# Kernel optimization log

Measured on AMD Instinct MI355X. Metric: run time of the kernel, lower is better.

## Reference

```python
import jax, jax.numpy as jnp
import numpy as np

B, S, D = 8, 1024, 512          # batch, seq_len, embed_dim
H = 8                            # num_heads
KD = D                           # key_dim = embed_dim (per source)
DM = H * KD                      # internal d_model = 4096
FF = 2048                        # dense_dim
EPS = 1e-3                       # keras LayerNormalization default epsilon


def glorot(key, shape):
    fan_in, fan_out = shape[0], shape[1]
    lim = np.sqrt(6.0 / (fan_in + fan_out)).astype(np.float32)
    return jax.random.uniform(key, shape, jnp.float32, -lim, lim)


def setup_inputs() -> dict:
    key = jax.random.key(0)
    ks = jax.random.split(key, 8)
    return {
        "inputs": jax.random.normal(ks[0], (B, S, D), jnp.float32),
        "w_q": glorot(ks[1], (D, DM)), "b_q": jnp.zeros((DM,), jnp.float32),
        "w_k": glorot(ks[2], (D, DM)), "b_k": jnp.zeros((DM,), jnp.float32),
        "w_v": glorot(ks[3], (D, DM)), "b_v": jnp.zeros((DM,), jnp.float32),
        "w_o": glorot(ks[4], (DM, D)), "b_o": jnp.zeros((D,), jnp.float32),
        "w1": glorot(ks[5], (D, FF)), "b1": jnp.zeros((FF,), jnp.float32),
        "w2": glorot(ks[6], (FF, D)), "b2": jnp.zeros((D,), jnp.float32),
        "g1": jnp.ones((D,), jnp.float32), "beta1": jnp.zeros((D,), jnp.float32),
        "g2": jnp.ones((D,), jnp.float32), "beta2": jnp.zeros((D,), jnp.float32),
    }


def _layernorm(x, gamma, beta):
    mu = jnp.mean(x, axis=-1, keepdims=True)
    var = jnp.mean(jnp.square(x - mu), axis=-1, keepdims=True)
    return (x - mu) * jax.lax.rsqrt(var + EPS) * gamma + beta


def reference(inputs, w_q, b_q, w_k, b_k, w_v, b_v, w_o, b_o,
              w1, b1, w2, b2, g1, beta1, g2, beta2):
    # --- custom multi-head self-attention ---
    q = (inputs @ w_q + b_q).reshape(B, S, H, KD)   # [B,S,H,KD]
    k = (inputs @ w_k + b_k).reshape(B, S, H, KD)
    v = (inputs @ w_v + b_v).reshape(B, S, H, KD)
    scale = jnp.sqrt(jnp.float32(KD))
    scores = jnp.einsum("bqhd,bkhd->bhqk", q, k) / scale   # [B,H,S,S]
    attn = jax.nn.softmax(scores, axis=-1)
    ctx = jnp.einsum("bhqk,bkhd->bqhd", attn, v).reshape(B, S, DM)
    attn_out = ctx @ w_o + b_o                               # [B,S,D]
    # --- residual + LN 1 ---
    proj_in = _layernorm(inputs + attn_out, g1, beta1)
    # --- FFN ---
    ffn = jax.nn.relu(proj_in @ w1 + b1) @ w2 + b2
    # --- residual + LN 2 ---
    return _layernorm(proj_in + ffn, g2, beta2)
```

## Files before the change

kernel.cpp:

```cpp
#include <hip/hip_runtime.h>
#include <stdint.h>

typedef __bf16 bf16_t;
typedef bf16_t bf16x8 __attribute__((ext_vector_type(8)));
typedef float floatx4 __attribute__((ext_vector_type(4)));

__device__ __forceinline__ unsigned short f2bf(float f) {
  union { float f; uint32_t u; } v; v.f = f;
  return (unsigned short)((v.u + 0x7fffu + ((v.u >> 16) & 1u)) >> 16);
}

#define GLD16(g, l)                                                            \
  __builtin_amdgcn_global_load_lds(                                            \
      (const __attribute__((address_space(1))) void*)(g),                      \
      (__attribute__((address_space(3))) void*)(l), 16, 0, 0)

template <int BIAS_MODE, bool RELU, bool OUT_BF16, bool HAS_RESID>
__global__ __launch_bounds__(256) void gemm_bt(
    const unsigned short* __restrict__ A, const unsigned short* __restrict__ Bt,
    void* __restrict__ C, const float* __restrict__ bias,
    const float* __restrict__ resid, int K, int lda, int ldb, int ldc,
    long sA, long sB, long sC, long sR) {
  __shared__ unsigned short As[128 * 64];
  __shared__ unsigned short Bs[128 * 64];
  const int tid = threadIdx.x;
  const int lane = tid & 63;
  const int wave = tid >> 6;
  const unsigned short* Ab = A + blockIdx.z * sA + (long)blockIdx.y * 128 * lda;
  const unsigned short* Bb = Bt + blockIdx.z * sB + (long)blockIdx.x * 128 * ldb;
  const int wm = (wave & 1) << 6;
  const int wn = (wave >> 1) << 6;

  floatx4 acc[4][4] = {};

  const int sr = tid >> 3;
  const int sc = tid & 7;

  for (int kt = 0; kt < K; kt += 64) {
#pragma unroll
    for (int i = 0; i < 4; ++i) {
      int r = sr + i * 32;
      int gc = sc ^ (r & 7);
      GLD16(Ab + (long)r * lda + kt + gc * 8, As + (i * 256 + wave * 64) * 8);
    }
#pragma unroll
    for (int i = 0; i < 4; ++i) {
      int r = sr + i * 32;
      int gc = sc ^ (r & 7);
      GLD16(Bb + (long)r * ldb + kt + gc * 8, Bs + (i * 256 + wave * 64) * 8);
    }
    __syncthreads();
#pragma unroll
    for (int ks = 0; ks < 2; ++ks) {
      bf16x8 af[4], bfr[4];
#pragma unroll
      for (int i = 0; i < 4; ++i) {
        int row = wm + i * 16 + (lane & 15);
        int ch = (ks * 4 + (lane >> 4)) ^ (row & 7);
        af[i] = *(const bf16x8*)(As + row * 64 + ch * 8);
      }
#pragma unroll
      for (int j = 0; j < 4; ++j) {
        int row = wn + j * 16 + (lane & 15);
        int ch = (ks * 4 + (lane >> 4)) ^ (row & 7);
        bfr[j] = *(const bf16x8*)(Bs + row * 64 + ch * 8);
      }
#pragma unroll
      for (int i = 0; i < 4; ++i)
#pragma unroll
        for (int j = 0; j < 4; ++j)
          acc[i][j] = __builtin_amdgcn_mfma_f32_16x16x32_bf16(af[i], bfr[j],
                                                              acc[i][j], 0, 0, 0);
    }
    __syncthreads();
  }

  const int rl = (lane >> 4) << 2;
  const int cl = lane & 15;
#pragma unroll
  for (int i = 0; i < 4; ++i) {
#pragma unroll
    for (int j = 0; j < 4; ++j) {
#pragma unroll
      for (int rg = 0; rg < 4; ++rg) {
        int row = (blockIdx.y << 7) + wm + i * 16 + rl + rg;
        int col = (blockIdx.x << 7) + wn + j * 16 + cl;
        float v = acc[i][j][rg];
        if (BIAS_MODE == 1) v += bias[col];
        if (BIAS_MODE == 2) v += bias[row];
        if (HAS_RESID) v += resid[blockIdx.z * sR + (long)row * ldc + col];
        if (RELU) v = fmaxf(v, 0.0f);
        long idx = blockIdx.z * sC + (long)row * ldc + col;
        if (OUT_BF16)
          ((unsigned short*)C)[idx] = f2bf(v);
        else
          ((float*)C)[idx] = v;
      }
    }
  }
}

__global__ __launch_bounds__(512, 2) void attn(
    const unsigned short* __restrict__ qk, const unsigned short* __restrict__ vt,
    unsigned short* __restrict__ ctx) {
  __shared__ unsigned short ldsK[2][32 * 512];
  __shared__ unsigned short ldsV[2][32 * 512];
  __shared__ unsigned short ldsP[128 * 40];
  __shared__ float ldsL[128];

  const int tid = threadIdx.x;
  const int lane = tid & 63;
  const int wave = tid >> 6;
  const int quad = lane >> 4;
  const int l15 = lane & 15;
  const int b = blockIdx.x >> 3;
  const int h = blockIdx.x & 7;
  const int qblk = blockIdx.y << 7;
  const float cs = 0.044194173824159216f * 1.4426950408889634f;

  bf16x8 qf[16];
  {
    const unsigned short* qp =
        qk + (long)(b * 1024 + qblk + wave * 16 + l15) * 8192 + h * 512 +
        (quad << 3);
#pragma unroll
    for (int ks = 0; ks < 16; ++ks) qf[ks] = *(const bf16x8*)(qp + ks * 32);
  }

  floatx4 o[32];
#pragma unroll
  for (int i = 0; i < 32; ++i) o[i] = floatx4{0.f, 0.f, 0.f, 0.f};
  floatx4 l_i = floatx4{0.f, 0.f, 0.f, 0.f};

  const int st_d = lane >> 2;
  const int st_kc = ((lane & 3) - (lane >> 3)) & 3;

  {
#pragma unroll
    for (int i = 0; i < 4; ++i) {
      int r = i * 8 + wave;
      int gc = (lane & ~7) | ((lane ^ r) & 7);
      GLD16(qk + (long)(b * 1024 + r) * 8192 + 4096 + h * 512 + gc * 8,
            ldsK[0] + r * 512);
    }
#pragma unroll
    for (int i = 0; i < 4; ++i) {
      int j = i * 8 + wave;
      GLD16(vt + (long)(b * 4096 + h * 512 + j * 16 + st_d) * 1024 + st_kc * 8,
            ldsV[0] + j * 512);
    }
  }
  __syncthreads();

  for (int kt = 0; kt < 32; ++kt) {
    const unsigned short* kb = ldsK[kt & 1];
    const unsigned short* vb = ldsV[kt & 1];
    if (kt + 1 < 32) {
#pragma unroll
      for (int i = 0; i < 4; ++i) {
        int r = i * 8 + wave;
        int gc = (lane & ~7) | ((lane ^ r) & 7);
        GLD16(qk + (long)(b * 1024 + (kt + 1) * 32 + r) * 8192 + 4096 +
                  h * 512 + gc * 8,
              ldsK[(kt + 1) & 1] + r * 512);
      }
#pragma unroll
      for (int i = 0; i < 4; ++i) {
        int j = i * 8 + wave;
        GLD16(vt + (long)(b * 4096 + h * 512 + j * 16 + st_d) * 1024 +
                  (kt + 1) * 32 + st_kc * 8,
              ldsV[(kt + 1) & 1] + j * 512);
      }
    }

    floatx4 s0 = floatx4{0.f, 0.f, 0.f, 0.f}, s1 = floatx4{0.f, 0.f, 0.f, 0.f};
#pragma unroll
    for (int ks = 0; ks < 16; ++ks) {
      int ch = ks * 4 + quad;
      int sw = (ch & ~7) | ((ch ^ l15) & 7);
      bf16x8 k0 = *(const bf16x8*)(kb + l15 * 512 + sw * 8);
      bf16x8 k1 = *(const bf16x8*)(kb + (16 + l15) * 512 + sw * 8);
      s0 = __builtin_amdgcn_mfma_f32_16x16x32_bf16(qf[ks], k0, s0, 0, 0, 0);
      s1 = __builtin_amdgcn_mfma_f32_16x16x32_bf16(qf[ks], k1, s1, 0, 0, 0);
    }

    {
      unsigned short* pw = ldsP + wave * 16 * 40;
      const int rb = quad << 2;
#pragma unroll
      for (int r = 0; r < 4; ++r) {
        float e0 = __builtin_amdgcn_exp2f(s0[r] * cs);
        float e1 = __builtin_amdgcn_exp2f(s1[r] * cs);
        l_i[r] += e0 + e1;
        pw[(rb + r) * 40 + l15] = f2bf(e0);
        pw[(rb + r) * 40 + 16 + l15] = f2bf(e1);
      }
    }
    asm volatile("s_waitcnt lgkmcnt(0)\n\ts_barrier" ::: "memory");

#pragma unroll
    for (int half = 0; half < 2; ++half) {
      bf16x8 pf[4];
#pragma unroll
      for (int q4 = 0; q4 < 4; ++q4)
        pf[q4] = *(const bf16x8*)(ldsP + ((half * 4 + q4) * 16 + l15) * 40 +
                                  (quad << 3));
#pragma unroll
      for (int db = 0; db < 4; ++db) {
        int n = wave * 4 + db;
        bf16x8 vf = *(const bf16x8*)(
            vb + n * 512 + (l15 * 4 + ((quad + (l15 >> 1)) & 3)) * 8);
#pragma unroll
        for (int q4 = 0; q4 < 4; ++q4)
          o[(half * 4 + q4) * 4 + db] = __builtin_amdgcn_mfma_f32_16x16x32_bf16(
              pf[q4], vf, o[(half * 4 + q4) * 4 + db], 0, 0, 0);
      }
    }
    __syncthreads();
  }

#pragma unroll
  for (int r = 0; r < 4; ++r) {
    float rs = l_i[r];
    rs += __shfl_xor(rs, 1);
    rs += __shfl_xor(rs, 2);
    rs += __shfl_xor(rs, 4);
    rs += __shfl_xor(rs, 8);
    if (l15 == 0) ldsL[wave * 16 + (quad << 2) + r] = rs;
  }
  __syncthreads();

#pragma unroll
  for (int qb = 0; qb < 8; ++qb) {
    floatx4 lv = *(const floatx4*)(ldsL + qb * 16 + (quad << 2));
    floatx4 inv;
#pragma unroll
    for (int r = 0; r < 4; ++r) inv[r] = 1.0f / lv[r];
#pragma unroll
    for (int db = 0; db < 4; ++db) {
#pragma unroll
      for (int r = 0; r < 4; ++r) {
        long row = (long)(b * 1024 + qblk + qb * 16 + (quad << 2) + r);
        ctx[row * 4096 + h * 512 + wave * 64 + db * 16 + l15] =
            f2bf(o[qb * 4 + db][r] * inv[r]);
      }
    }
  }
}

template <bool WB>
__global__ __launch_bounds__(256) void ln_reduce(
    const float* __restrict__ p, long sP, const float* __restrict__ bias,
    const float* __restrict__ resid, const float* __restrict__ gamma,
    const float* __restrict__ beta, float* __restrict__ of,
    unsigned short* __restrict__ ob) {
  const long row = blockIdx.x;
  const int c = threadIdx.x * 2;
  const float2 a0 = ((const float2*)(p + row * 512))[threadIdx.x];
  const float2 a1 = ((const float2*)(p + sP + row * 512))[threadIdx.x];
  const float2 a2 = ((const float2*)(p + 2 * sP + row * 512))[threadIdx.x];
  const float2 a3 = ((const float2*)(p + 3 * sP + row * 512))[threadIdx.x];
  const float2 rv = ((const float2*)(resid + row * 512))[threadIdx.x];
  const float x0 = a0.x + a1.x + a2.x + a3.x + bias[c] + rv.x;
  const float x1 = a0.y + a1.y + a2.y + a3.y + bias[c + 1] + rv.y;
  float s = x0 + x1;
  float ss = x0 * x0 + x1 * x1;
#pragma unroll
  for (int d = 1; d < 64; d <<= 1) {
    s += __shfl_xor(s, d);
    ss += __shfl_xor(ss, d);
  }
  __shared__ float ps[4], pq[4];
  const int wave = threadIdx.x >> 6;
  if ((threadIdx.x & 63) == 0) {
    ps[wave] = s;
    pq[wave] = ss;
  }
  __syncthreads();
  s = ps[0] + ps[1] + ps[2] + ps[3];
  ss = pq[0] + pq[1] + pq[2] + pq[3];
  const float mu = s * (1.0f / 512.0f);
  const float rstd = rsqrtf(ss * (1.0f / 512.0f) - mu * mu + 1e-3f);
  const float y0 = (x0 - mu) * rstd * gamma[c] + beta[c];
  const float y1 = (x1 - mu) * rstd * gamma[c + 1] + beta[c + 1];
  ((float2*)(of + row * 512))[threadIdx.x] = make_float2(y0, y1);
  if (WB) {
    ushort2 o2;
    o2.x = f2bf(y0);
    o2.y = f2bf(y1);
    ((ushort2*)(ob + row * 512))[threadIdx.x] = o2;
  }
}

__global__ __launch_bounds__(256) void cast_bf16(const float* __restrict__ in,
                                                 unsigned short* __restrict__ out,
                                                 int n) {
  int i = (blockIdx.x * 256 + threadIdx.x) * 4;
  if (i < n) {
    float4 v = *(const float4*)(in + i);
    ushort4 o;
    o.x = f2bf(v.x);
    o.y = f2bf(v.y);
    o.z = f2bf(v.z);
    o.w = f2bf(v.w);
    *(ushort4*)(out + i) = o;
  }
}

__global__ __launch_bounds__(256) void transpose_cast(const float* __restrict__ in,
                                                      unsigned short* __restrict__ out,
                                                      int R, int C) {
  __shared__ float tile[32][33];
  const int tx = threadIdx.x & 31, ty = threadIdx.x >> 5;
  const int c0 = blockIdx.x * 32, r0 = blockIdx.y * 32;
#pragma unroll
  for (int i = 0; i < 4; ++i)
    tile[ty + i * 8][tx] = in[(long)(r0 + ty + i * 8) * C + c0 + tx];
  __syncthreads();
#pragma unroll
  for (int i = 0; i < 4; ++i)
    out[(long)(c0 + ty + i * 8) * R + r0 + tx] = f2bf(tile[tx][ty + i * 8]);
}

extern "C" void kernel_launch(void* const* d_in, const int* in_sizes, int n_in,
                              void* d_out, int out_size, void* d_ws,
                              size_t ws_size, hipStream_t stream) {
  const float* x = (const float*)d_in[0];
  const float* w_q = (const float*)d_in[1];
  const float* b_q = (const float*)d_in[2];
  const float* w_k = (const float*)d_in[3];
  const float* b_k = (const float*)d_in[4];
  const float* w_v = (const float*)d_in[5];
  const float* b_v = (const float*)d_in[6];
  const float* w_o = (const float*)d_in[7];
  const float* b_o = (const float*)d_in[8];
  const float* w1 = (const float*)d_in[9];
  const float* b1 = (const float*)d_in[10];
  const float* w2 = (const float*)d_in[11];
  const float* b2 = (const float*)d_in[12];
  const float* g1 = (const float*)d_in[13];
  const float* be1 = (const float*)d_in[14];
  const float* g2 = (const float*)d_in[15];
  const float* be2 = (const float*)d_in[16];
  float* out = (float*)d_out;

  char* ws = (char*)d_ws;
  size_t off = 0;
  auto alloc = [&](size_t n) {
    char* p = ws + off;
    off += (n + 255) & ~(size_t)255;
    return p;
  };
  unsigned short* xb = (unsigned short*)alloc(8192ll * 512 * 2);
  unsigned short* wqk_t = (unsigned short*)alloc(8192ll * 512 * 2);
  unsigned short* wv_t = (unsigned short*)alloc(4096ll * 512 * 2);
  unsigned short* wo_t = (unsigned short*)alloc(512ll * 4096 * 2);
  unsigned short* w1_t = (unsigned short*)alloc(2048ll * 512 * 2);
  unsigned short* w2_t = (unsigned short*)alloc(512ll * 2048 * 2);
  float* bqk = (float*)alloc(8192ll * 4);
  unsigned short* qkb = (unsigned short*)alloc(4096ll * 8192 * 2);
  unsigned short* vtb = (unsigned short*)alloc(4ll * 4096 * 1024 * 2);
  unsigned short* ctxf = (unsigned short*)alloc(8192ll * 4096 * 2);
  float* proj = (float*)alloc(8192ll * 512 * 4);
  unsigned short* projb = xb;
  unsigned short* h1 = qkb;
  float* pOP = (float*)qkb;
  float* pF2 = (float*)ctxf;

  hipMemcpyAsync(bqk, b_q, 4096 * 4, hipMemcpyDeviceToDevice, stream);
  hipMemcpyAsync(bqk + 4096, b_k, 4096 * 4, hipMemcpyDeviceToDevice, stream);

  cast_bf16<<<4096, 256, 0, stream>>>(x, xb, 8192 * 512);
  transpose_cast<<<dim3(128, 16), 256, 0, stream>>>(w_q, wqk_t, 512, 4096);
  transpose_cast<<<dim3(128, 16), 256, 0, stream>>>(w_k, wqk_t + 4096ll * 512, 512, 4096);
  transpose_cast<<<dim3(128, 16), 256, 0, stream>>>(w_v, wv_t, 512, 4096);
  transpose_cast<<<dim3(16, 128), 256, 0, stream>>>(w_o, wo_t, 4096, 512);
  transpose_cast<<<dim3(64, 16), 256, 0, stream>>>(w1, w1_t, 512, 2048);
  transpose_cast<<<dim3(16, 64), 256, 0, stream>>>(w2, w2_t, 2048, 512);

  for (int g = 0; g < 2; ++g) {
    const unsigned short* xg = xb + (long)g * 4096 * 512;
    gemm_bt<1, false, true, false><<<dim3(64, 32, 1), 256, 0, stream>>>(
        xg, wqk_t, qkb, bqk, nullptr, 512, 512, 512, 8192, 0, 0, 0, 0);
    gemm_bt<2, false, true, false><<<dim3(8, 32, 4), 256, 0, stream>>>(
        wv_t, xg, vtb, b_v, nullptr, 512, 512, 512, 1024, 0, 1024ll * 512,
        4096ll * 1024, 0);
    attn<<<dim3(32, 8), 512, 0, stream>>>(qkb, vtb, ctxf + (long)g * 4096 * 4096);
  }
  gemm_bt<0, false, false, false><<<dim3(4, 64, 4), 256, 0, stream>>>(
      ctxf, wo_t, pOP, nullptr, nullptr, 1024, 4096, 4096, 512, 1024, 1024,
      8192ll * 512, 0);
  ln_reduce<true><<<8192, 256, 0, stream>>>(pOP, 8192ll * 512, b_o, x, g1, be1,
                                            proj, projb);
  gemm_bt<1, true, true, false><<<dim3(16, 64, 1), 256, 0, stream>>>(
      projb, w1_t, h1, b1, nullptr, 512, 512, 512, 2048, 0, 0, 0, 0);
  gemm_bt<0, false, false, false><<<dim3(4, 64, 4), 256, 0, stream>>>(
      h1, w2_t, pF2, nullptr, nullptr, 512, 2048, 2048, 512, 512, 512,
      8192ll * 512, 0);
  ln_reduce<false><<<8192, 256, 0, stream>>>(pF2, 8192ll * 512, b2, proj, g2,
                                             be2, out, nullptr);
}
```

Before: 561.2 us.

## Halve attention query tile and single-buffer K/V with staggered loads

The attention kernel now handles 64 query rows per block with 4 waves instead of 128 rows with 8 waves, which doubles the grid, and each wave covers 128 output columns. The K/V double buffers become single buffers. V for the current tile loads while QK^T runs, and K for the next tile loads during the PV step after the barrier, so the LDS footprint roughly halves. The aim is more resident blocks and better load overlap. In exchange, each K/V tile is reused by half as many queries, so global K/V traffic doubles, and the added barriers may expose latency.

```diff
diff --git a/kernel.cpp b/kernel.cpp
--- a/kernel.cpp
+++ b/kernel.cpp
@@ -100,13 +100,13 @@
   }
 }
 
-__global__ __launch_bounds__(512, 2) void attn(
+__global__ __launch_bounds__(256, 2) void attn(
     const unsigned short* __restrict__ qk, const unsigned short* __restrict__ vt,
     unsigned short* __restrict__ ctx) {
-  __shared__ unsigned short ldsK[2][32 * 512];
-  __shared__ unsigned short ldsV[2][32 * 512];
-  __shared__ unsigned short ldsP[128 * 40];
-  __shared__ float ldsL[128];
+  __shared__ unsigned short ldsK[32 * 512];
+  __shared__ unsigned short ldsV[32 * 512];
+  __shared__ unsigned short ldsP[64 * 40];
+  __shared__ float ldsL[64];
 
   const int tid = threadIdx.x;
   const int lane = tid & 63;
@@ -115,7 +115,7 @@
   const int l15 = lane & 15;
   const int b = blockIdx.x >> 3;
   const int h = blockIdx.x & 7;
-  const int qblk = blockIdx.y << 7;
+  const int qblk = blockIdx.y << 6;
   const float cs = 0.044194173824159216f * 1.4426950408889634f;
 
   bf16x8 qf[16];
@@ -137,40 +137,23 @@
 
   {
 #pragma unroll
-    for (int i = 0; i < 4; ++i) {
-      int r = i * 8 + wave;
+    for (int i = 0; i < 8; ++i) {
+      int r = i * 4 + wave;
       int gc = (lane & ~7) | ((lane ^ r) & 7);
       GLD16(qk + (long)(b * 1024 + r) * 8192 + 4096 + h * 512 + gc * 8,
-            ldsK[0] + r * 512);
-    }
-#pragma unroll
-    for (int i = 0; i < 4; ++i) {
-      int j = i * 8 + wave;
-      GLD16(vt + (long)(b * 4096 + h * 512 + j * 16 + st_d) * 1024 + st_kc * 8,
-            ldsV[0] + j * 512);
-    }
-  }
-  __syncthreads();
+            ldsK + r * 512);
+    }
+  }
 
   for (int kt = 0; kt < 32; ++kt) {
-    const unsigned short* kb = ldsK[kt & 1];
-    const unsigned short* vb = ldsV[kt & 1];
-    if (kt + 1 < 32) {
-#pragma unroll
-      for (int i = 0; i < 4; ++i) {
-        int r = i * 8 + wave;
-        int gc = (lane & ~7) | ((lane ^ r) & 7);
-        GLD16(qk + (long)(b * 1024 + (kt + 1) * 32 + r) * 8192 + 4096 +
-                  h * 512 + gc * 8,
-              ldsK[(kt + 1) & 1] + r * 512);
-      }
-#pragma unroll
-      for (int i = 0; i < 4; ++i) {
-        int j = i * 8 + wave;
-        GLD16(vt + (long)(b * 4096 + h * 512 + j * 16 + st_d) * 1024 +
-                  (kt + 1) * 32 + st_kc * 8,
-              ldsV[(kt + 1) & 1] + j * 512);
-      }
+    __syncthreads();
+
+#pragma unroll
+    for (int i = 0; i < 8; ++i) {
+      int j = i * 4 + wave;
+      GLD16(vt + (long)(b * 4096 + h * 512 + j * 16 + st_d) * 1024 + kt * 32 +
+                st_kc * 8,
+            ldsV + j * 512);
     }
 
     floatx4 s0 = floatx4{0.f, 0.f, 0.f, 0.f}, s1 = floatx4{0.f, 0.f, 0.f, 0.f};
@@ -178,8 +161,8 @@
     for (int ks = 0; ks < 16; ++ks) {
       int ch = ks * 4 + quad;
       int sw = (ch & ~7) | ((ch ^ l15) & 7);
-      bf16x8 k0 = *(const bf16x8*)(kb + l15 * 512 + sw * 8);
-      bf16x8 k1 = *(const bf16x8*)(kb + (16 + l15) * 512 + sw * 8);
+      bf16x8 k0 = *(const bf16x8*)(ldsK + l15 * 512 + sw * 8);
+      bf16x8 k1 = *(const bf16x8*)(ldsK + (16 + l15) * 512 + sw * 8);
       s0 = __builtin_amdgcn_mfma_f32_16x16x32_bf16(qf[ks], k0, s0, 0, 0, 0);
       s1 = __builtin_amdgcn_mfma_f32_16x16x32_bf16(qf[ks], k1, s1, 0, 0, 0);
     }
@@ -196,27 +179,33 @@
         pw[(rb + r) * 40 + 16 + l15] = f2bf(e1);
       }
     }
-    asm volatile("s_waitcnt lgkmcnt(0)\n\ts_barrier" ::: "memory");
-
-#pragma unroll
-    for (int half = 0; half < 2; ++half) {
-      bf16x8 pf[4];
+    asm volatile("s_waitcnt vmcnt(0) lgkmcnt(0)\n\ts_barrier" ::: "memory");
+
+    if (kt + 1 < 32) {
+#pragma unroll
+      for (int i = 0; i < 8; ++i) {
+        int r = i * 4 + wave;
+        int gc = (lane & ~7) | ((lane ^ r) & 7);
+        GLD16(qk + (long)(b * 1024 + (kt + 1) * 32 + r) * 8192 + 4096 +
+                  h * 512 + gc * 8,
+              ldsK + r * 512);
+      }
+    }
+
+    bf16x8 pf[4];
+#pragma unroll
+    for (int q4 = 0; q4 < 4; ++q4)
+      pf[q4] = *(const bf16x8*)(ldsP + (q4 * 16 + l15) * 40 + (quad << 3));
+#pragma unroll
+    for (int db = 0; db < 8; ++db) {
+      int n = wave * 8 + db;
+      bf16x8 vf = *(const bf16x8*)(
+          ldsV + n * 512 + (l15 * 4 + ((quad + (l15 >> 1)) & 3)) * 8);
 #pragma unroll
       for (int q4 = 0; q4 < 4; ++q4)
-        pf[q4] = *(const bf16x8*)(ldsP + ((half * 4 + q4) * 16 + l15) * 40 +
-                                  (quad << 3));
-#pragma unroll
-      for (int db = 0; db < 4; ++db) {
-        int n = wave * 4 + db;
-        bf16x8 vf = *(const bf16x8*)(
-            vb + n * 512 + (l15 * 4 + ((quad + (l15 >> 1)) & 3)) * 8);
-#pragma unroll
-        for (int q4 = 0; q4 < 4; ++q4)
-          o[(half * 4 + q4) * 4 + db] = __builtin_amdgcn_mfma_f32_16x16x32_bf16(
-              pf[q4], vf, o[(half * 4 + q4) * 4 + db], 0, 0, 0);
-      }
-    }
-    __syncthreads();
+        o[q4 * 8 + db] = __builtin_amdgcn_mfma_f32_16x16x32_bf16(
+            pf[q4], vf, o[q4 * 8 + db], 0, 0, 0);
+    }
   }
 
 #pragma unroll
@@ -231,18 +220,18 @@
   __syncthreads();
 
 #pragma unroll
-  for (int qb = 0; qb < 8; ++qb) {
-    floatx4 lv = *(const floatx4*)(ldsL + qb * 16 + (quad << 2));
+  for (int q4 = 0; q4 < 4; ++q4) {
+    floatx4 lv = *(const floatx4*)(ldsL + q4 * 16 + (quad << 2));
     floatx4 inv;
 #pragma unroll
     for (int r = 0; r < 4; ++r) inv[r] = 1.0f / lv[r];
 #pragma unroll
-    for (int db = 0; db < 4; ++db) {
+    for (int db = 0; db < 8; ++db) {
 #pragma unroll
       for (int r = 0; r < 4; ++r) {
-        long row = (long)(b * 1024 + qblk + qb * 16 + (quad << 2) + r);
-        ctx[row * 4096 + h * 512 + wave * 64 + db * 16 + l15] =
-            f2bf(o[qb * 4 + db][r] * inv[r]);
+        long row = (long)(b * 1024 + qblk + q4 * 16 + (quad << 2) + r);
+        ctx[row * 4096 + h * 512 + wave * 128 + db * 16 + l15] =
+            f2bf(o[q4 * 8 + db][r] * inv[r]);
       }
     }
   }
@@ -385,7 +374,7 @@
     gemm_bt<2, false, true, false><<<dim3(8, 32, 4), 256, 0, stream>>>(
         wv_t, xg, vtb, b_v, nullptr, 512, 512, 512, 1024, 0, 1024ll * 512,
         4096ll * 1024, 0);
-    attn<<<dim3(32, 8), 512, 0, stream>>>(qkb, vtb, ctxf + (long)g * 4096 * 4096);
+    attn<<<dim3(32, 16), 256, 0, stream>>>(qkb, vtb, ctxf + (long)g * 4096 * 4096);
   }
   gemm_bt<0, false, false, false><<<dim3(4, 64, 4), 256, 0, stream>>>(
       ctxf, wo_t, pOP, nullptr, nullptr, 1024, 4096, 4096, 512, 1024, 1024,
```

New measurement: 572.1 us. Within noise of the previous version (+2.0%).

## Replace 128x128 GEMM with double-buffered 256x256 tile kernel using 8 waves

Applied to the files above, without the earlier changes.

Swaps the GEMM kernel for one that computes 256x256 output tiles with 512 threads. It double-buffers LDS so global-to-LDS loads for tile t+2 overlap the MFMA work on tile t, and raises wave priority around the MFMA bursts. Larger tiles raise arithmetic intensity and cut global traffic per FLOP. In exchange each block uses 128KB of LDS and more accumulator registers, and grids are smaller, which may lower occupancy and CU fill for the smaller GEMMs.

```diff
diff --git a/kernel.cpp b/kernel.cpp
--- a/kernel.cpp
+++ b/kernel.cpp
@@ -15,80 +15,115 @@
       (const __attribute__((address_space(1))) void*)(g),                      \
       (__attribute__((address_space(3))) void*)(l), 16, 0, 0)
 
-template <int BIAS_MODE, bool RELU, bool OUT_BF16, bool HAS_RESID>
-__global__ __launch_bounds__(256) void gemm_bt(
+template <int BIAS_MODE, bool RELU, bool OUT_BF16>
+__global__ __launch_bounds__(512, 2) void gemm256(
     const unsigned short* __restrict__ A, const unsigned short* __restrict__ Bt,
-    void* __restrict__ C, const float* __restrict__ bias,
-    const float* __restrict__ resid, int K, int lda, int ldb, int ldc,
-    long sA, long sB, long sC, long sR) {
-  __shared__ unsigned short As[128 * 64];
-  __shared__ unsigned short Bs[128 * 64];
+    void* __restrict__ C, const float* __restrict__ bias, int K, int lda,
+    int ldb, int ldc, long sA, long sB, long sC) {
+  __shared__ __align__(16) unsigned short As[2][256 * 64];
+  __shared__ __align__(16) unsigned short Bs[2][256 * 64];
   const int tid = threadIdx.x;
   const int lane = tid & 63;
   const int wave = tid >> 6;
-  const unsigned short* Ab = A + blockIdx.z * sA + (long)blockIdx.y * 128 * lda;
-  const unsigned short* Bb = Bt + blockIdx.z * sB + (long)blockIdx.x * 128 * ldb;
-  const int wm = (wave & 1) << 6;
+  const int quad = lane >> 4;
+  const int l15 = lane & 15;
+  const unsigned short* Ab = A + blockIdx.z * sA + (long)blockIdx.y * 256 * lda;
+  const unsigned short* Bb = Bt + blockIdx.z * sB + (long)blockIdx.x * 256 * ldb;
+  const int wm = (wave & 1) << 7;
   const int wn = (wave >> 1) << 6;
 
-  floatx4 acc[4][4] = {};
+  floatx4 acc[8][4] = {};
 
   const int sr = tid >> 3;
   const int sc = tid & 7;
-
-  for (int kt = 0; kt < K; kt += 64) {
+  const int NT = K >> 6;
+
+  auto stage = [&](int t, int buf) {
+    const int kt = t << 6;
 #pragma unroll
     for (int i = 0; i < 4; ++i) {
-      int r = sr + i * 32;
+      int r = sr + i * 64;
       int gc = sc ^ (r & 7);
-      GLD16(Ab + (long)r * lda + kt + gc * 8, As + (i * 256 + wave * 64) * 8);
+      GLD16(Ab + (long)r * lda + kt + gc * 8,
+            &As[buf][(i * 64 + (wave << 3)) * 64]);
     }
 #pragma unroll
     for (int i = 0; i < 4; ++i) {
-      int r = sr + i * 32;
+      int r = sr + i * 64;
       int gc = sc ^ (r & 7);
-      GLD16(Bb + (long)r * ldb + kt + gc * 8, Bs + (i * 256 + wave * 64) * 8);
-    }
-    __syncthreads();
-#pragma unroll
-    for (int ks = 0; ks < 2; ++ks) {
-      bf16x8 af[4], bfr[4];
-#pragma unroll
-      for (int i = 0; i < 4; ++i) {
-        int row = wm + i * 16 + (lane & 15);
-        int ch = (ks * 4 + (lane >> 4)) ^ (row & 7);
-        af[i] = *(const bf16x8*)(As + row * 64 + ch * 8);
-      }
-#pragma unroll
-      for (int j = 0; j < 4; ++j) {
-        int row = wn + j * 16 + (lane & 15);
-        int ch = (ks * 4 + (lane >> 4)) ^ (row & 7);
-        bfr[j] = *(const bf16x8*)(Bs + row * 64 + ch * 8);
-      }
-#pragma unroll
-      for (int i = 0; i < 4; ++i)
-#pragma unroll
-        for (int j = 0; j < 4; ++j)
-          acc[i][j] = __builtin_amdgcn_mfma_f32_16x16x32_bf16(af[i], bfr[j],
-                                                              acc[i][j], 0, 0, 0);
-    }
-    __syncthreads();
-  }
-
-  const int rl = (lane >> 4) << 2;
-  const int cl = lane & 15;
-#pragma unroll
-  for (int i = 0; i < 4; ++i) {
+      GLD16(Bb + (long)r * ldb + kt + gc * 8,
+            &Bs[buf][(i * 64 + (wave << 3)) * 64]);
+    }
+  };
+
+  stage(0, 0);
+  stage(1, 1);
+  asm volatile("s_waitcnt vmcnt(8)\n\ts_barrier" ::: "memory");
+
+  int cur = 0;
+  for (int t = 0; t < NT; ++t) {
+    const unsigned short* Ap = As[cur];
+    const unsigned short* Bp = Bs[cur];
+#pragma unroll
+    for (int ih = 0; ih < 2; ++ih) {
+      bf16x8 aF[4][2];
+#pragma unroll
+      for (int i4 = 0; i4 < 4; ++i4)
+#pragma unroll
+        for (int ks = 0; ks < 2; ++ks) {
+          int row = wm + ih * 64 + i4 * 16 + l15;
+          int sw = (ks * 4 + quad) ^ (row & 7);
+          aF[i4][ks] = *(const bf16x8*)(Ap + row * 64 + sw * 8);
+        }
+#pragma unroll
+      for (int jh = 0; jh < 2; ++jh) {
+        bf16x8 bF[2][2];
+#pragma unroll
+        for (int j2 = 0; j2 < 2; ++j2)
+#pragma unroll
+          for (int ks = 0; ks < 2; ++ks) {
+            int row = wn + jh * 32 + j2 * 16 + l15;
+            int sw = (ks * 4 + quad) ^ (row & 7);
+            bF[j2][ks] = *(const bf16x8*)(Bp + row * 64 + sw * 8);
+          }
+        __builtin_amdgcn_s_setprio(1);
+#pragma unroll
+        for (int j2 = 0; j2 < 2; ++j2)
+#pragma unroll
+          for (int i4 = 0; i4 < 4; ++i4)
+#pragma unroll
+            for (int ks = 0; ks < 2; ++ks)
+              acc[ih * 4 + i4][jh * 2 + j2] =
+                  __builtin_amdgcn_mfma_f32_16x16x32_bf16(
+                      aF[i4][ks], bF[j2][ks], acc[ih * 4 + i4][jh * 2 + j2],
+                      0, 0, 0);
+        __builtin_amdgcn_s_setprio(0);
+      }
+    }
+    if (t == NT - 1) break;
+    asm volatile("s_waitcnt lgkmcnt(0)\n\ts_barrier" ::: "memory");
+    if (t + 2 < NT) {
+      stage(t + 2, cur);
+      asm volatile("s_waitcnt vmcnt(8)\n\ts_barrier" ::: "memory");
+    } else {
+      asm volatile("s_waitcnt vmcnt(0)\n\ts_barrier" ::: "memory");
+    }
+    cur ^= 1;
+  }
+
+  const int rl = quad << 2;
+  const int cl = l15;
+#pragma unroll
+  for (int i = 0; i < 8; ++i) {
 #pragma unroll
     for (int j = 0; j < 4; ++j) {
 #pragma unroll
       for (int rg = 0; rg < 4; ++rg) {
-        int row = (blockIdx.y << 7) + wm + i * 16 + rl + rg;
-        int col = (blockIdx.x << 7) + wn + j * 16 + cl;
+        int row = (blockIdx.y << 8) + wm + i * 16 + rl + rg;
+        int col = (blockIdx.x << 8) + wn + j * 16 + cl;
         float v = acc[i][j][rg];
         if (BIAS_MODE == 1) v += bias[col];
         if (BIAS_MODE == 2) v += bias[row];
-        if (HAS_RESID) v += resid[blockIdx.z * sR + (long)row * ldc + col];
         if (RELU) v = fmaxf(v, 0.0f);
         long idx = blockIdx.z * sC + (long)row * ldc + col;
         if (OUT_BF16)
@@ -380,23 +415,22 @@
 
   for (int g = 0; g < 2; ++g) {
     const unsigned short* xg = xb + (long)g * 4096 * 512;
-    gemm_bt<1, false, true, false><<<dim3(64, 32, 1), 256, 0, stream>>>(
-        xg, wqk_t, qkb, bqk, nullptr, 512, 512, 512, 8192, 0, 0, 0, 0);
-    gemm_bt<2, false, true, false><<<dim3(8, 32, 4), 256, 0, stream>>>(
-        wv_t, xg, vtb, b_v, nullptr, 512, 512, 512, 1024, 0, 1024ll * 512,
-        4096ll * 1024, 0);
+    gemm256<1, false, true><<<dim3(32, 16, 1), 512, 0, stream>>>(
+        xg, wqk_t, qkb, bqk, 512, 512, 512, 8192, 0, 0, 0);
+    gemm256<2, false, true><<<dim3(4, 16, 4), 512, 0, stream>>>(
+        wv_t, xg, vtb, b_v, 512, 512, 512, 1024, 0, 1024ll * 512,
+        4096ll * 1024);
     attn<<<dim3(32, 8), 512, 0, stream>>>(qkb, vtb, ctxf + (long)g * 4096 * 4096);
   }
-  gemm_bt<0, false, false, false><<<dim3(4, 64, 4), 256, 0, stream>>>(
-      ctxf, wo_t, pOP, nullptr, nullptr, 1024, 4096, 4096, 512, 1024, 1024,
-      8192ll * 512, 0);
+  gemm256<0, false, false><<<dim3(2, 32, 4), 512, 0, stream>>>(
+      ctxf, wo_t, pOP, nullptr, 1024, 4096, 4096, 512, 1024, 1024,
+      8192ll * 512);
   ln_reduce<true><<<8192, 256, 0, stream>>>(pOP, 8192ll * 512, b_o, x, g1, be1,
                                             proj, projb);
-  gemm_bt<1, true, true, false><<<dim3(16, 64, 1), 256, 0, stream>>>(
-      projb, w1_t, h1, b1, nullptr, 512, 512, 512, 2048, 0, 0, 0, 0);
-  gemm_bt<0, false, false, false><<<dim3(4, 64, 4), 256, 0, stream>>>(
-      h1, w2_t, pF2, nullptr, nullptr, 512, 2048, 2048, 512, 512, 512,
-      8192ll * 512, 0);
+  gemm256<1, true, true><<<dim3(8, 32, 1), 512, 0, stream>>>(
+      projb, w1_t, h1, b1, 512, 512, 512, 2048, 0, 0, 0);
+  gemm256<0, false, false><<<dim3(2, 32, 4), 512, 0, stream>>>(
+      h1, w2_t, pF2, nullptr, 512, 2048, 2048, 512, 512, 512, 8192ll * 512);
   ln_reduce<false><<<8192, 256, 0, stream>>>(pF2, 8192ll * 512, b2, proj, g2,
                                              be2, out, nullptr);
 }
```

Result: faster. 507.2 us (-9.6%).
